# Kernel tuning notes

Hardware: AMD Instinct MI355X
Metric: run time of the kernel (lower is better)

## Reference

```python
import jax, jax.numpy as jnp
import numpy as np

B, S, H, E = 32, 2048, 1024, 1024
NEG = -10000000000.0


def setup_inputs() -> dict:
    key = jax.random.key(0)
    ks = jax.random.split(key, 8)
    scale = 1.0 / np.sqrt(H)
    return {
        "hidden": jax.random.normal(ks[0], (B, H), jnp.float32),
        "encoder_outputs": jax.random.normal(ks[1], (B, S, E), jnp.float32),
        "mask": jax.random.randint(ks[2], (B, S), 0, 2, jnp.int32),
        "W_h": jax.random.normal(ks[3], (H, H), jnp.float32) * scale,
        "b_h": jax.random.normal(ks[4], (H,), jnp.float32) * scale,
        "W_e": jax.random.normal(ks[5], (E, H), jnp.float32) * scale,
        "b_e": jax.random.normal(ks[6], (H,), jnp.float32) * scale,
        "v": jax.random.normal(ks[7], (H,), jnp.float32) * scale,
    }


def reference(hidden, encoder_outputs, mask, W_h, b_h, W_e, b_e, v):
    # hidden proj: (B,H) -> (B,1,H); encoder proj: (B,S,E) -> (B,S,H)
    h_proj = (hidden @ W_h + b_h)[:, None, :]
    e_proj = jnp.einsum("bse,eh->bsh", encoder_outputs, W_e) + b_e
    energy = jnp.tanh(h_proj + e_proj)                      # (B,S,H)
    attention = jnp.einsum("bsh,h->bs", energy, v)          # (B,S)
    attention = jnp.where(mask == 0, NEG, attention)
    attention_weights = jax.nn.softmax(attention, axis=1)   # (B,S)
    context = jnp.einsum("bs,bse->be", attention_weights, encoder_outputs)
    return (context, attention_weights)
```

## Files before the change

### kernel.cpp

```cpp
#include <hip/hip_runtime.h>

#define NEGV -10000000000.0f

typedef _Float16 half8 __attribute__((ext_vector_type(8)));
typedef float f32x4 __attribute__((ext_vector_type(4)));

__device__ __forceinline__ void gld16(const void* g, void* l) {
  __builtin_amdgcn_global_load_lds((const __attribute__((address_space(1))) void*)g,
                                   (__attribute__((address_space(3))) void*)l,
                                   16, 0, 0);
}

__device__ __forceinline__ float fast_tanh(float x) {
  const float e = __expf(2.0f * x);
  return 1.0f - 2.0f * __builtin_amdgcn_rcpf(e + 1.0f);
}

__global__ __launch_bounds__(256) void prep_kernel(
    const float* __restrict__ enc, _Float16* __restrict__ enc16,
    const float* __restrict__ We, _Float16* __restrict__ W16T,
    const float* __restrict__ hidden, const float* __restrict__ W_h,
    const float* __restrict__ b_h, const float* __restrict__ b_e,
    float* __restrict__ hpb) {
  __shared__ float tile[32][33];
  const int bid = blockIdx.x;
  const int tid = threadIdx.x;

  if (bid < 128) {
    const int b = bid >> 2;
    const int h = ((bid & 3) << 8) | tid;
    const float* hb = hidden + b * 1024;
    float a0 = 0.f, a1 = 0.f, a2 = 0.f, a3 = 0.f;
    #pragma unroll 4
    for (int k = 0; k < 1024; k += 4) {
      a0 = fmaf(hb[k + 0], W_h[(size_t)(k + 0) * 1024 + h], a0);
      a1 = fmaf(hb[k + 1], W_h[(size_t)(k + 1) * 1024 + h], a1);
      a2 = fmaf(hb[k + 2], W_h[(size_t)(k + 2) * 1024 + h], a2);
      a3 = fmaf(hb[k + 3], W_h[(size_t)(k + 3) * 1024 + h], a3);
    }
    hpb[b * 1024 + h] = b_h[h] + b_e[h] + ((a0 + a1) + (a2 + a3));
  } else if (bid < 128 + 1024) {
    const int tb = bid - 128;
    const int n0 = (tb & 31) << 5, k0 = (tb >> 5) << 5;
    const int tx = tid & 31, ty = tid >> 5;
    #pragma unroll
    for (int i = 0; i < 4; ++i) {
      const int r = ty + (i << 3);
      tile[r][tx] = We[(size_t)(k0 + r) * 1024 + n0 + tx];
    }
    __syncthreads();
    #pragma unroll
    for (int i = 0; i < 4; ++i) {
      const int r = ty + (i << 3);
      W16T[(size_t)(n0 + r) * 1024 + k0 + tx] = (_Float16)tile[tx][r];
    }
  } else {
    const size_t base = ((size_t)(bid - 1152) * 256 + tid) * 8;
    const float4 x = *(const float4*)(enc + base);
    const float4 y = *(const float4*)(enc + base + 4);
    half8 h;
    h[0] = (_Float16)x.x; h[1] = (_Float16)x.y; h[2] = (_Float16)x.z; h[3] = (_Float16)x.w;
    h[4] = (_Float16)y.x; h[5] = (_Float16)y.y; h[6] = (_Float16)y.z; h[7] = (_Float16)y.w;
    *(half8*)(enc16 + base) = h;
  }
}

__global__ __launch_bounds__(512, 2) void attn_gemm8_kernel(
    const _Float16* __restrict__ enc16, const _Float16* __restrict__ W16T,
    const float* __restrict__ hpb, const float* __restrict__ v,
    const int* __restrict__ mask, float* __restrict__ logits) {
  __shared__ __align__(16) _Float16 Abuf[3][256 * 32];
  __shared__ __align__(16) _Float16 Bbuf[3][256 * 32];
  __shared__ float hp_s[1024];
  __shared__ float vh_s[1024];
  __shared__ float red[1024];

  const int tid = threadIdx.x;
  const int wid = tid >> 6;
  const int lane = tid & 63;
  const int l15 = lane & 15;
  const int qq = lane >> 4;
  const int wr = wid >> 2;
  const int wc = wid & 3;
  const int m0 = blockIdx.x << 8;
  const int b = blockIdx.x >> 3;

  for (int i = tid; i < 1024; i += 512) {
    hp_s[i] = hpb[(b << 10) + i];
    vh_s[i] = v[i];
  }

  const int r0 = tid >> 2;
  const int r1 = r0 + 128;
  const int g0 = tid & 3;
  const int sc = (g0 ^ ((r0 >> 1) & 3)) << 4;
  const int ldsoff0 = (wid << 10);
  const int ldsoff1 = (wid << 10) + 8192;

  const char* encb = (const char*)(enc16 + (size_t)m0 * 1024);
  const char* wb0 = (const char*)W16T;

  auto stageA = [&](int buf, int t) {
    const int colb = ((t & 31) << 6) + sc;
    char* base = (char*)(&Abuf[buf][0]);
    gld16(encb + (size_t)r0 * 2048 + colb, base + ldsoff0);
    gld16(encb + (size_t)r1 * 2048 + colb, base + ldsoff1);
  };
  auto stageB = [&](int buf, int t) {
    const char* wb = wb0 + ((size_t)(t >> 5) << 19);
    const int colb = ((t & 31) << 6) + sc;
    char* base = (char*)(&Bbuf[buf][0]);
    gld16(wb + (size_t)r0 * 2048 + colb, base + ldsoff0);
    gld16(wb + (size_t)r1 * 2048 + colb, base + ldsoff1);
  };

  int aoff[2][4], boff[4];
  #pragma unroll
  for (int mh = 0; mh < 2; ++mh)
    #pragma unroll
    for (int mi = 0; mi < 4; ++mi) {
      const int row = (wr << 7) + (mh << 6) + (mi << 4) + l15;
      aoff[mh][mi] = (row << 6) + ((qq ^ ((row >> 1) & 3)) << 4);
    }
  #pragma unroll
  for (int ni = 0; ni < 4; ++ni) {
    const int np = (wc << 6) + (ni << 4) + l15;
    boff[ni] = (np << 6) + ((qq ^ ((np >> 1) & 3)) << 4);
  }

  f32x4 acc[8][4];
  float rowsum[8][4];
  #pragma unroll
  for (int mi = 0; mi < 8; ++mi)
    #pragma unroll
    for (int j = 0; j < 4; ++j) {
      acc[mi][j] = (f32x4){0.f, 0.f, 0.f, 0.f};
      rowsum[mi][j] = 0.f;
    }

  stageA(0, 0); stageB(0, 0);
  stageA(1, 1); stageB(1, 1);
  __syncthreads();

  int bi = 0;
  #pragma unroll 1
  for (int t = 0; t < 128; ++t) {
    const int bi2 = (bi >= 1) ? bi - 1 : bi + 2;
    const char* A = (const char*)(&Abuf[bi][0]);
    const char* B = (const char*)(&Bbuf[bi][0]);
    half8 a0[4], a1[4], bf[4];

    #pragma unroll
    for (int mi = 0; mi < 4; ++mi) a0[mi] = *(const half8*)(A + aoff[0][mi]);
    #pragma unroll
    for (int ni = 0; ni < 4; ++ni) bf[ni] = *(const half8*)(B + boff[ni]);
    #pragma unroll
    for (int mi = 0; mi < 4; ++mi) a1[mi] = *(const half8*)(A + aoff[1][mi]);

    if (t < 126) { stageA(bi2, t + 2); stageB(bi2, t + 2); }

    __builtin_amdgcn_s_setprio(1);
    #pragma unroll
    for (int mi = 0; mi < 4; ++mi)
      #pragma unroll
      for (int ni = 0; ni < 4; ++ni)
        acc[mi][ni] = __builtin_amdgcn_mfma_f32_16x16x32_f16(a0[mi], bf[ni], acc[mi][ni], 0, 0, 0);
    #pragma unroll
    for (int mi = 0; mi < 4; ++mi)
      #pragma unroll
      for (int ni = 0; ni < 4; ++ni)
        acc[4 + mi][ni] = __builtin_amdgcn_mfma_f32_16x16x32_f16(a1[mi], bf[ni], acc[4 + mi][ni], 0, 0, 0);
    __builtin_amdgcn_s_setprio(0);

    if (t < 126) asm volatile("s_waitcnt vmcnt(4)" ::: "memory");
    else         asm volatile("s_waitcnt vmcnt(0)" ::: "memory");
    __builtin_amdgcn_s_barrier();

    if ((t & 31) == 31) {
      const int nt = t >> 5;
      const int hb = (nt << 8) + (wc << 6);
      #pragma unroll
      for (int ni = 0; ni < 4; ++ni) {
        const int h = hb + (ni << 4) + l15;
        const float hv = hp_s[h];
        const float vv = vh_s[h];
        #pragma unroll
        for (int mi = 0; mi < 8; ++mi) {
          #pragma unroll
          for (int r = 0; r < 4; ++r)
            rowsum[mi][r] += fast_tanh(acc[mi][ni][r] + hv) * vv;
          acc[mi][ni] = (f32x4){0.f, 0.f, 0.f, 0.f};
        }
      }
    }
    bi = (bi >= 2) ? 0 : bi + 1;
  }

  #pragma unroll
  for (int mi = 0; mi < 8; ++mi)
    #pragma unroll
    for (int r = 0; r < 4; ++r) {
      float s = rowsum[mi][r];
      s += __shfl_xor(s, 1);
      s += __shfl_xor(s, 2);
      s += __shfl_xor(s, 4);
      s += __shfl_xor(s, 8);
      rowsum[mi][r] = s;
    }
  __syncthreads();
  if (l15 == 0) {
    #pragma unroll
    for (int mi = 0; mi < 8; ++mi)
      #pragma unroll
      for (int r = 0; r < 4; ++r) {
        const int row = (wr << 7) + (mi << 4) + (qq << 2) + r;
        red[(row << 2) + wc] = rowsum[mi][r];
      }
  }
  __syncthreads();
  if (tid < 256) {
    const float s = red[tid << 2] + red[(tid << 2) + 1] + red[(tid << 2) + 2] + red[(tid << 2) + 3];
    const int m = m0 + tid;
    logits[m] = (mask[(b << 11) + (m & 2047)] == 0) ? NEGV : s;
  }
}

__global__ void softmax_kernel(const float* __restrict__ logits, float* __restrict__ wout) {
  __shared__ float red[4];
  const int b = blockIdx.x, tid = threadIdx.x;
  const int wid = tid >> 6, lane = tid & 63;
  const float* lb = logits + b * 2048;
  float x[8];
  #pragma unroll
  for (int j = 0; j < 8; ++j) x[j] = lb[tid + j * 256];
  float m = x[0];
  #pragma unroll
  for (int j = 1; j < 8; ++j) m = fmaxf(m, x[j]);
  #pragma unroll
  for (int off = 32; off > 0; off >>= 1) m = fmaxf(m, __shfl_xor(m, off));
  if (lane == 0) red[wid] = m;
  __syncthreads();
  m = fmaxf(fmaxf(red[0], red[1]), fmaxf(red[2], red[3]));
  __syncthreads();
  float e[8];
  float s = 0.f;
  #pragma unroll
  for (int j = 0; j < 8; ++j) { e[j] = expf(x[j] - m); s += e[j]; }
  #pragma unroll
  for (int off = 32; off > 0; off >>= 1) s += __shfl_xor(s, off);
  if (lane == 0) red[wid] = s;
  __syncthreads();
  s = red[0] + red[1] + red[2] + red[3];
  const float inv = 1.0f / s;
  #pragma unroll
  for (int j = 0; j < 8; ++j) wout[b * 2048 + tid + j * 256] = e[j] * inv;
}

__global__ void context16_kernel(const _Float16* __restrict__ enc16,
                                 const float* __restrict__ wout, float* __restrict__ ctx) {
  const int b = blockIdx.x >> 4;
  const int ch = blockIdx.x & 15;
  const int tl = threadIdx.x & 127;
  const int sh = threadIdx.x >> 7;
  float a[8] = {0.f, 0.f, 0.f, 0.f, 0.f, 0.f, 0.f, 0.f};
  #pragma unroll 1
  for (int i = 0; i < 64; ++i) {
    const int s = (ch << 7) + (i << 1) + sh;
    const float w = wout[(b << 11) + s];
    const half8 r = *(const half8*)(enc16 + (((size_t)(b << 11) + s) << 10) + (tl << 3));
    #pragma unroll
    for (int j = 0; j < 8; ++j) a[j] = fmaf(w, (float)r[j], a[j]);
  }
  float* c = ctx + (b << 10) + (tl << 3);
  #pragma unroll
  for (int j = 0; j < 8; ++j) atomicAdd(c + j, a[j]);
}

extern "C" void kernel_launch(void* const* d_in, const int* in_sizes, int n_in,
                              void* d_out, int out_size, void* d_ws, size_t ws_size,
                              hipStream_t stream) {
  const float* hidden = (const float*)d_in[0];
  const float* enc    = (const float*)d_in[1];
  const int*   mask   = (const int*)d_in[2];
  const float* W_h    = (const float*)d_in[3];
  const float* b_h    = (const float*)d_in[4];
  const float* W_e    = (const float*)d_in[5];
  const float* b_e    = (const float*)d_in[6];
  const float* v      = (const float*)d_in[7];

  float* ctx  = (float*)d_out;
  float* wout = (float*)d_out + 32 * 1024;

  char* ws = (char*)d_ws;
  const size_t ENC16_BYTES = 134217728ULL;
  _Float16* enc16 = (_Float16*)ws;
  _Float16* W16T  = (_Float16*)(ws + ENC16_BYTES);
  float* hpb      = (float*)(ws + ENC16_BYTES + 2097152);
  float* logits   = (float*)(ws + ENC16_BYTES + 2097152 + 131072);

  hipMemsetAsync(ctx, 0, 32 * 1024 * sizeof(float), stream);
  hipLaunchKernelGGL(prep_kernel, dim3(1152 + 32768), dim3(256), 0, stream,
                     enc, enc16, W_e, W16T, hidden, W_h, b_h, b_e, hpb);
  hipLaunchKernelGGL(attn_gemm8_kernel, dim3(256), dim3(512), 0, stream,
                     enc16, W16T, hpb, v, mask, logits);
  hipLaunchKernelGGL(softmax_kernel, dim3(32), dim3(256), 0, stream, logits, wout);
  hipLaunchKernelGGL(context16_kernel, dim3(512), dim3(256), 0, stream, enc16, wout, ctx);
}
```

Baseline: 283.5 us.

## Load GEMM B operand directly from global into registers, bypassing LDS

Removes the LDS staging buffer for the transposed weight tile. Each wave now loads its own B fragments straight from global memory into registers, one iteration ahead, and swaps them in after the MFMA block. The aim is to cut LDS footprint and LDS read traffic. In exchange, waves sharing a column redundantly load the same weights. The register copy of prefetched data may also force an early wait on the global loads, exposing global latency inside the main loop.

```diff
diff --git a/kernel.cpp b/kernel.cpp
--- a/kernel.cpp
+++ b/kernel.cpp
@@ -70,7 +70,6 @@
     const float* __restrict__ hpb, const float* __restrict__ v,
     const int* __restrict__ mask, float* __restrict__ logits) {
   __shared__ __align__(16) _Float16 Abuf[3][256 * 32];
-  __shared__ __align__(16) _Float16 Bbuf[3][256 * 32];
   __shared__ float hp_s[1024];
   __shared__ float vh_s[1024];
   __shared__ float red[1024];
@@ -106,15 +105,19 @@
     gld16(encb + (size_t)r0 * 2048 + colb, base + ldsoff0);
     gld16(encb + (size_t)r1 * 2048 + colb, base + ldsoff1);
   };
-  auto stageB = [&](int buf, int t) {
-    const char* wb = wb0 + ((size_t)(t >> 5) << 19);
-    const int colb = ((t & 31) << 6) + sc;
-    char* base = (char*)(&Bbuf[buf][0]);
-    gld16(wb + (size_t)r0 * 2048 + colb, base + ldsoff0);
-    gld16(wb + (size_t)r1 * 2048 + colb, base + ldsoff1);
+
+  int bofG[4];
+  #pragma unroll
+  for (int ni = 0; ni < 4; ++ni)
+    bofG[ni] = (((wc << 6) + (ni << 4) + l15) << 11) + (qq << 4);
+
+  auto loadB = [&](half8* dst, int t) {
+    const char* wb = wb0 + ((size_t)(t >> 5) << 19) + ((t & 31) << 6);
+    #pragma unroll
+    for (int ni = 0; ni < 4; ++ni) dst[ni] = *(const half8*)(wb + bofG[ni]);
   };
 
-  int aoff[2][4], boff[4];
+  int aoff[2][4];
   #pragma unroll
   for (int mh = 0; mh < 2; ++mh)
     #pragma unroll
@@ -122,11 +125,6 @@
       const int row = (wr << 7) + (mh << 6) + (mi << 4) + l15;
       aoff[mh][mi] = (row << 6) + ((qq ^ ((row >> 1) & 3)) << 4);
     }
-  #pragma unroll
-  for (int ni = 0; ni < 4; ++ni) {
-    const int np = (wc << 6) + (ni << 4) + l15;
-    boff[ni] = (np << 6) + ((qq ^ ((np >> 1) & 3)) << 4);
-  }
 
   f32x4 acc[8][4];
   float rowsum[8][4];
@@ -138,8 +136,10 @@
       rowsum[mi][j] = 0.f;
     }
 
-  stageA(0, 0); stageB(0, 0);
-  stageA(1, 1); stageB(1, 1);
+  half8 bf[4], bfn[4];
+  stageA(0, 0);
+  stageA(1, 1);
+  loadB(bf, 0);
   __syncthreads();
 
   int bi = 0;
@@ -147,17 +147,15 @@
   for (int t = 0; t < 128; ++t) {
     const int bi2 = (bi >= 1) ? bi - 1 : bi + 2;
     const char* A = (const char*)(&Abuf[bi][0]);
-    const char* B = (const char*)(&Bbuf[bi][0]);
-    half8 a0[4], a1[4], bf[4];
+    half8 a0[4], a1[4];
 
     #pragma unroll
     for (int mi = 0; mi < 4; ++mi) a0[mi] = *(const half8*)(A + aoff[0][mi]);
     #pragma unroll
-    for (int ni = 0; ni < 4; ++ni) bf[ni] = *(const half8*)(B + boff[ni]);
-    #pragma unroll
     for (int mi = 0; mi < 4; ++mi) a1[mi] = *(const half8*)(A + aoff[1][mi]);
 
-    if (t < 126) { stageA(bi2, t + 2); stageB(bi2, t + 2); }
+    if (t < 126) stageA(bi2, t + 2);
+    if (t < 127) loadB(bfn, t + 1);
 
     __builtin_amdgcn_s_setprio(1);
     #pragma unroll
@@ -172,7 +170,12 @@
         acc[4 + mi][ni] = __builtin_amdgcn_mfma_f32_16x16x32_f16(a1[mi], bf[ni], acc[4 + mi][ni], 0, 0, 0);
     __builtin_amdgcn_s_setprio(0);
 
-    if (t < 126) asm volatile("s_waitcnt vmcnt(4)" ::: "memory");
+    if (t < 127) {
+      #pragma unroll
+      for (int ni = 0; ni < 4; ++ni) bf[ni] = bfn[ni];
+    }
+
+    if (t < 126) asm volatile("s_waitcnt vmcnt(6)" ::: "memory");
     else         asm volatile("s_waitcnt vmcnt(0)" ::: "memory");
     __builtin_amdgcn_s_barrier();
 
```

Result: slower. 364.0 us (+28.4%).

## Shrink attention GEMM block to 128-row tiles with 4 warps, 512 blocks

Applied to the files above, without the earlier changes.

Reworks the fused attention-logit GEMM from 256x256 tiles with 8 waves per block to 128x256 tiles with 4 waves. The grid doubles to 512 blocks, which fills more CUs on the 256-CU MI355X than the previous 256 blocks. LDS use also drops: the A buffer is smaller, v is stored in fp16, and the reduction scratch reuses Abuf. In exchange, each block reloads the full W tile for half the rows, so W traffic per unit of work doubles and per-block arithmetic intensity falls. The vmcnt wait count is raised to match the larger number of loads per thread.

```diff
diff --git a/kernel.cpp b/kernel.cpp
--- a/kernel.cpp
+++ b/kernel.cpp
@@ -65,53 +65,56 @@
   }
 }
 
-__global__ __launch_bounds__(512, 2) void attn_gemm8_kernel(
+__global__ __launch_bounds__(256, 2) void attn_gemm8_kernel(
     const _Float16* __restrict__ enc16, const _Float16* __restrict__ W16T,
     const float* __restrict__ hpb, const float* __restrict__ v,
     const int* __restrict__ mask, float* __restrict__ logits) {
-  __shared__ __align__(16) _Float16 Abuf[3][256 * 32];
+  __shared__ __align__(16) _Float16 Abuf[3][128 * 32];
   __shared__ __align__(16) _Float16 Bbuf[3][256 * 32];
   __shared__ float hp_s[1024];
-  __shared__ float vh_s[1024];
-  __shared__ float red[1024];
+  __shared__ _Float16 vh_s[1024];
 
   const int tid = threadIdx.x;
   const int wid = tid >> 6;
   const int lane = tid & 63;
   const int l15 = lane & 15;
   const int qq = lane >> 4;
-  const int wr = wid >> 2;
-  const int wc = wid & 3;
-  const int m0 = blockIdx.x << 8;
-  const int b = blockIdx.x >> 3;
-
-  for (int i = tid; i < 1024; i += 512) {
+  const int wc = wid;
+  const int m0 = blockIdx.x << 7;
+  const int b = blockIdx.x >> 4;
+
+  for (int i = tid; i < 1024; i += 256) {
     hp_s[i] = hpb[(b << 10) + i];
-    vh_s[i] = v[i];
-  }
-
-  const int r0 = tid >> 2;
-  const int r1 = r0 + 128;
+    vh_s[i] = (_Float16)v[i];
+  }
+
+  const int rA = tid >> 2;
   const int g0 = tid & 3;
-  const int sc = (g0 ^ ((r0 >> 1) & 3)) << 4;
-  const int ldsoff0 = (wid << 10);
-  const int ldsoff1 = (wid << 10) + 8192;
+  const int ldsoff = (wid << 10);
 
   const char* encb = (const char*)(enc16 + (size_t)m0 * 1024);
   const char* wb0 = (const char*)W16T;
 
   auto stageA = [&](int buf, int t) {
-    const int colb = ((t & 31) << 6) + sc;
-    char* base = (char*)(&Abuf[buf][0]);
-    gld16(encb + (size_t)r0 * 2048 + colb, base + ldsoff0);
-    gld16(encb + (size_t)r1 * 2048 + colb, base + ldsoff1);
+    const int colb = (t & 31) << 6;
+    char* base = (char*)(&Abuf[buf][0]) + ldsoff;
+    #pragma unroll
+    for (int i = 0; i < 2; ++i) {
+      const int row = rA + (i << 6);
+      const int col = colb + (((g0 ^ ((row >> 1) & 3))) << 4);
+      gld16(encb + (size_t)row * 2048 + col, base + (i << 12));
+    }
   };
   auto stageB = [&](int buf, int t) {
     const char* wb = wb0 + ((size_t)(t >> 5) << 19);
-    const int colb = ((t & 31) << 6) + sc;
-    char* base = (char*)(&Bbuf[buf][0]);
-    gld16(wb + (size_t)r0 * 2048 + colb, base + ldsoff0);
-    gld16(wb + (size_t)r1 * 2048 + colb, base + ldsoff1);
+    const int colb = (t & 31) << 6;
+    char* base = (char*)(&Bbuf[buf][0]) + ldsoff;
+    #pragma unroll
+    for (int i = 0; i < 4; ++i) {
+      const int np = rA + (i << 6);
+      const int col = colb + (((g0 ^ ((np >> 1) & 3))) << 4);
+      gld16(wb + (size_t)np * 2048 + col, base + (i << 12));
+    }
   };
 
   int aoff[2][4], boff[4];
@@ -119,7 +122,7 @@
   for (int mh = 0; mh < 2; ++mh)
     #pragma unroll
     for (int mi = 0; mi < 4; ++mi) {
-      const int row = (wr << 7) + (mh << 6) + (mi << 4) + l15;
+      const int row = (mh << 6) + (mi << 4) + l15;
       aoff[mh][mi] = (row << 6) + ((qq ^ ((row >> 1) & 3)) << 4);
     }
   #pragma unroll
@@ -172,7 +175,7 @@
         acc[4 + mi][ni] = __builtin_amdgcn_mfma_f32_16x16x32_f16(a1[mi], bf[ni], acc[4 + mi][ni], 0, 0, 0);
     __builtin_amdgcn_s_setprio(0);
 
-    if (t < 126) asm volatile("s_waitcnt vmcnt(4)" ::: "memory");
+    if (t < 126) asm volatile("s_waitcnt vmcnt(6)" ::: "memory");
     else         asm volatile("s_waitcnt vmcnt(0)" ::: "memory");
     __builtin_amdgcn_s_barrier();
 
@@ -183,7 +186,7 @@
       for (int ni = 0; ni < 4; ++ni) {
         const int h = hb + (ni << 4) + l15;
         const float hv = hp_s[h];
-        const float vv = vh_s[h];
+        const float vv = (float)vh_s[h];
         #pragma unroll
         for (int mi = 0; mi < 8; ++mi) {
           #pragma unroll
@@ -207,18 +210,19 @@
       s += __shfl_xor(s, 8);
       rowsum[mi][r] = s;
     }
+  float* red = (float*)(&Abuf[0][0]);
   __syncthreads();
   if (l15 == 0) {
     #pragma unroll
     for (int mi = 0; mi < 8; ++mi)
       #pragma unroll
       for (int r = 0; r < 4; ++r) {
-        const int row = (wr << 7) + (mi << 4) + (qq << 2) + r;
+        const int row = (mi << 4) + (qq << 2) + r;
         red[(row << 2) + wc] = rowsum[mi][r];
       }
   }
   __syncthreads();
-  if (tid < 256) {
+  if (tid < 128) {
     const float s = red[tid << 2] + red[(tid << 2) + 1] + red[(tid << 2) + 2] + red[(tid << 2) + 3];
     const int m = m0 + tid;
     logits[m] = (mask[(b << 11) + (m & 2047)] == 0) ? NEGV : s;
@@ -301,7 +305,7 @@
   hipMemsetAsync(ctx, 0, 32 * 1024 * sizeof(float), stream);
   hipLaunchKernelGGL(prep_kernel, dim3(1152 + 32768), dim3(256), 0, stream,
                      enc, enc16, W_e, W16T, hidden, W_h, b_h, b_e, hpb);
-  hipLaunchKernelGGL(attn_gemm8_kernel, dim3(256), dim3(512), 0, stream,
+  hipLaunchKernelGGL(attn_gemm8_kernel, dim3(512), dim3(256), 0, stream,
                      enc16, W16T, hpb, v, mask, logits);
   hipLaunchKernelGGL(softmax_kernel, dim3(32), dim3(256), 0, stream, logits, wout);
   hipLaunchKernelGGL(context16_kernel, dim3(512), dim3(256), 0, stream, enc16, wout, ctx);
```

New measurement: 296.3 us. 1.05x slower.

## Fuse fp32-to-fp16 encoder conversion into GEMM A-tile staging, drop enc16 buffer

Applied to the files above, without the earlier changes.

Removes the separate pass that converted the whole encoder tensor to fp16 in workspace. The GEMM now loads fp32 encoder rows into registers, converts them, and writes them into the swizzled LDS A-tile one stage ahead. The context kernel reads fp32 encoder outputs directly. This avoids writing and re-reading a 128MB intermediate, but the GEMM's A-tile traffic doubles, the global-to-LDS async path for A is replaced by register staging, and the context kernel reads twice the bytes.

```diff
diff --git a/kernel.cpp b/kernel.cpp
--- a/kernel.cpp
+++ b/kernel.cpp
@@ -17,7 +17,6 @@
 }
 
 __global__ __launch_bounds__(256) void prep_kernel(
-    const float* __restrict__ enc, _Float16* __restrict__ enc16,
     const float* __restrict__ We, _Float16* __restrict__ W16T,
     const float* __restrict__ hidden, const float* __restrict__ W_h,
     const float* __restrict__ b_h, const float* __restrict__ b_e,
@@ -39,7 +38,7 @@
       a3 = fmaf(hb[k + 3], W_h[(size_t)(k + 3) * 1024 + h], a3);
     }
     hpb[b * 1024 + h] = b_h[h] + b_e[h] + ((a0 + a1) + (a2 + a3));
-  } else if (bid < 128 + 1024) {
+  } else {
     const int tb = bid - 128;
     const int n0 = (tb & 31) << 5, k0 = (tb >> 5) << 5;
     const int tx = tid & 31, ty = tid >> 5;
@@ -54,19 +53,11 @@
       const int r = ty + (i << 3);
       W16T[(size_t)(n0 + r) * 1024 + k0 + tx] = (_Float16)tile[tx][r];
     }
-  } else {
-    const size_t base = ((size_t)(bid - 1152) * 256 + tid) * 8;
-    const float4 x = *(const float4*)(enc + base);
-    const float4 y = *(const float4*)(enc + base + 4);
-    half8 h;
-    h[0] = (_Float16)x.x; h[1] = (_Float16)x.y; h[2] = (_Float16)x.z; h[3] = (_Float16)x.w;
-    h[4] = (_Float16)y.x; h[5] = (_Float16)y.y; h[6] = (_Float16)y.z; h[7] = (_Float16)y.w;
-    *(half8*)(enc16 + base) = h;
   }
 }
 
 __global__ __launch_bounds__(512, 2) void attn_gemm8_kernel(
-    const _Float16* __restrict__ enc16, const _Float16* __restrict__ W16T,
+    const float* __restrict__ enc32, const _Float16* __restrict__ W16T,
     const float* __restrict__ hpb, const float* __restrict__ v,
     const int* __restrict__ mask, float* __restrict__ logits) {
   __shared__ __align__(16) _Float16 Abuf[3][256 * 32];
@@ -93,22 +84,35 @@
   const int r0 = tid >> 2;
   const int r1 = r0 + 128;
   const int g0 = tid & 3;
-  const int sc = (g0 ^ ((r0 >> 1) & 3)) << 4;
+  const int swzd = (g0 ^ ((r0 >> 1) & 3)) << 4;
+  const int scB = swzd;
   const int ldsoff0 = (wid << 10);
   const int ldsoff1 = (wid << 10) + 8192;
 
-  const char* encb = (const char*)(enc16 + (size_t)m0 * 1024);
+  const float* encb = enc32 + (size_t)m0 * 1024;
   const char* wb0 = (const char*)W16T;
 
-  auto stageA = [&](int buf, int t) {
-    const int colb = ((t & 31) << 6) + sc;
-    char* base = (char*)(&Abuf[buf][0]);
-    gld16(encb + (size_t)r0 * 2048 + colb, base + ldsoff0);
-    gld16(encb + (size_t)r1 * 2048 + colb, base + ldsoff1);
+  f32x4 af[4];
+  auto issueA = [&](int t) {
+    const float* p0 = encb + (size_t)r0 * 1024 + ((t & 31) << 5) + (g0 << 3);
+    const float* p1 = encb + (size_t)r1 * 1024 + ((t & 31) << 5) + (g0 << 3);
+    af[0] = *(const f32x4*)p0; af[1] = *(const f32x4*)(p0 + 4);
+    af[2] = *(const f32x4*)p1; af[3] = *(const f32x4*)(p1 + 4);
+  };
+  auto writeA = [&](int buf) {
+    half8 h0, h1;
+    #pragma unroll
+    for (int j = 0; j < 4; ++j) {
+      h0[j] = (_Float16)af[0][j]; h0[4 + j] = (_Float16)af[1][j];
+      h1[j] = (_Float16)af[2][j]; h1[4 + j] = (_Float16)af[3][j];
+    }
+    char* Ab = (char*)(&Abuf[buf][0]);
+    *(half8*)(Ab + (r0 << 6) + swzd) = h0;
+    *(half8*)(Ab + (r1 << 6) + swzd) = h1;
   };
   auto stageB = [&](int buf, int t) {
     const char* wb = wb0 + ((size_t)(t >> 5) << 19);
-    const int colb = ((t & 31) << 6) + sc;
+    const int colb = ((t & 31) << 6) + scB;
     char* base = (char*)(&Bbuf[buf][0]);
     gld16(wb + (size_t)r0 * 2048 + colb, base + ldsoff0);
     gld16(wb + (size_t)r1 * 2048 + colb, base + ldsoff1);
@@ -138,14 +142,18 @@
       rowsum[mi][j] = 0.f;
     }
 
-  stageA(0, 0); stageB(0, 0);
-  stageA(1, 1); stageB(1, 1);
-  __syncthreads();
-
-  int bi = 0;
+  issueA(0);
+  stageB(0, 0); stageB(1, 1);
+  asm volatile("s_waitcnt vmcnt(4)" ::: "memory");
+  writeA(0);
+  issueA(1);
+  __syncthreads();
+
   #pragma unroll 1
   for (int t = 0; t < 128; ++t) {
-    const int bi2 = (bi >= 1) ? bi - 1 : bi + 2;
+    const int bi = t % 3;
+    const int bi1 = (bi >= 2) ? 0 : bi + 1;
+    const int bi2 = (bi1 >= 2) ? 0 : bi1 + 1;
     const char* A = (const char*)(&Abuf[bi][0]);
     const char* B = (const char*)(&Bbuf[bi][0]);
     half8 a0[4], a1[4], bf[4];
@@ -157,7 +165,8 @@
     #pragma unroll
     for (int mi = 0; mi < 4; ++mi) a1[mi] = *(const half8*)(A + aoff[1][mi]);
 
-    if (t < 126) { stageA(bi2, t + 2); stageB(bi2, t + 2); }
+    if (t < 127) writeA(bi1);
+    if (t < 126) { issueA(t + 2); stageB(bi2, t + 2); }
 
     __builtin_amdgcn_s_setprio(1);
     #pragma unroll
@@ -172,8 +181,9 @@
         acc[4 + mi][ni] = __builtin_amdgcn_mfma_f32_16x16x32_f16(a1[mi], bf[ni], acc[4 + mi][ni], 0, 0, 0);
     __builtin_amdgcn_s_setprio(0);
 
-    if (t < 126) asm volatile("s_waitcnt vmcnt(4)" ::: "memory");
+    if (t < 126) asm volatile("s_waitcnt vmcnt(6)" ::: "memory");
     else         asm volatile("s_waitcnt vmcnt(0)" ::: "memory");
+    asm volatile("s_waitcnt lgkmcnt(0)" ::: "memory");
     __builtin_amdgcn_s_barrier();
 
     if ((t & 31) == 31) {
@@ -193,7 +203,6 @@
         }
       }
     }
-    bi = (bi >= 2) ? 0 : bi + 1;
   }
 
   #pragma unroll
@@ -256,24 +265,27 @@
   for (int j = 0; j < 8; ++j) wout[b * 2048 + tid + j * 256] = e[j] * inv;
 }
 
-__global__ void context16_kernel(const _Float16* __restrict__ enc16,
-                                 const float* __restrict__ wout, float* __restrict__ ctx) {
+__global__ void context_kernel(const float* __restrict__ enc, const float* __restrict__ wout,
+                               float* __restrict__ ctx) {
   const int b = blockIdx.x >> 4;
   const int ch = blockIdx.x & 15;
-  const int tl = threadIdx.x & 127;
-  const int sh = threadIdx.x >> 7;
-  float a[8] = {0.f, 0.f, 0.f, 0.f, 0.f, 0.f, 0.f, 0.f};
-  #pragma unroll 1
-  for (int i = 0; i < 64; ++i) {
-    const int s = (ch << 7) + (i << 1) + sh;
-    const float w = wout[(b << 11) + s];
-    const half8 r = *(const half8*)(enc16 + (((size_t)(b << 11) + s) << 10) + (tl << 3));
-    #pragma unroll
-    for (int j = 0; j < 8; ++j) a[j] = fmaf(w, (float)r[j], a[j]);
-  }
-  float* c = ctx + (b << 10) + (tl << 3);
-  #pragma unroll
-  for (int j = 0; j < 8; ++j) atomicAdd(c + j, a[j]);
+  const int tid = threadIdx.x;
+  float ax = 0.f, ay = 0.f, az = 0.f, aw = 0.f;
+  const int s0 = ch * 128;
+  for (int i = 0; i < 128; ++i) {
+    const int s = s0 + i;
+    const float w = wout[b * 2048 + s];
+    const float4 r = *(const float4*)(enc + (size_t)(b * 2048 + s) * 1024 + tid * 4);
+    ax = fmaf(w, r.x, ax);
+    ay = fmaf(w, r.y, ay);
+    az = fmaf(w, r.z, az);
+    aw = fmaf(w, r.w, aw);
+  }
+  float* c = ctx + b * 1024 + tid * 4;
+  atomicAdd(c + 0, ax);
+  atomicAdd(c + 1, ay);
+  atomicAdd(c + 2, az);
+  atomicAdd(c + 3, aw);
 }
 
 extern "C" void kernel_launch(void* const* d_in, const int* in_sizes, int n_in,
@@ -292,17 +304,15 @@
   float* wout = (float*)d_out + 32 * 1024;
 
   char* ws = (char*)d_ws;
-  const size_t ENC16_BYTES = 134217728ULL;
-  _Float16* enc16 = (_Float16*)ws;
-  _Float16* W16T  = (_Float16*)(ws + ENC16_BYTES);
-  float* hpb      = (float*)(ws + ENC16_BYTES + 2097152);
-  float* logits   = (float*)(ws + ENC16_BYTES + 2097152 + 131072);
+  _Float16* W16T = (_Float16*)ws;
+  float* hpb     = (float*)(ws + 2097152);
+  float* logits  = (float*)(ws + 2097152 + 131072);
 
   hipMemsetAsync(ctx, 0, 32 * 1024 * sizeof(float), stream);
-  hipLaunchKernelGGL(prep_kernel, dim3(1152 + 32768), dim3(256), 0, stream,
-                     enc, enc16, W_e, W16T, hidden, W_h, b_h, b_e, hpb);
+  hipLaunchKernelGGL(prep_kernel, dim3(1152), dim3(256), 0, stream,
+                     W_e, W16T, hidden, W_h, b_h, b_e, hpb);
   hipLaunchKernelGGL(attn_gemm8_kernel, dim3(256), dim3(512), 0, stream,
-                     enc16, W16T, hpb, v, mask, logits);
+                     enc, W16T, hpb, v, mask, logits);
   hipLaunchKernelGGL(softmax_kernel, dim3(32), dim3(256), 0, stream, logits, wout);
-  hipLaunchKernelGGL(context16_kernel, dim3(512), dim3(256), 0, stream, enc16, wout, ctx);
-}
+  hipLaunchKernelGGL(context_kernel, dim3(512), dim3(256), 0, stream, enc, wout, ctx);
+}
```

Result: faster. 257.6 us (median of 2 runs) (-9.1%).
